# Kernel optimization log

Hardware: AMD Instinct MI355X
Metric: run time of the kernel (lower is better)

## Reference

```python
import jax, jax.numpy as jnp
import numpy as np

B, IN_DIM, N, L = 8, 2, 512, 64
D_MODEL = 32
D_FF = 32          # must equal D_MODEL: output_bn is BatchNorm2d(d_model) applied to skip
DEPTH = 3          # blocks=3 * layers=1; dilation resets to 1 each block -> all dilations = 1
KS = 2             # temporal kernel size
EPS = 1e-5         # BatchNorm eps


def setup_inputs() -> dict:
    key = jax.random.key(0)
    ks = jax.random.split(key, 16)
    s = 0.1  # weight scale for numeric sanity
    x = jax.random.normal(ks[0], (B, IN_DIM, N, L), jnp.float32)
    a = jax.random.uniform(ks[1], (N, N), jnp.float32)
    adj = a / a.sum(axis=1, keepdims=True)  # row-stochastic diffusion matrix
    return {
        "x": x,
        "adj": adj,
        "Wstart": jax.random.normal(ks[2], (D_MODEL, IN_DIM), jnp.float32) * s,
        "bstart": jnp.zeros((D_MODEL,), jnp.float32),
        "Wf": jax.random.normal(ks[3], (DEPTH, D_MODEL, D_MODEL, KS), jnp.float32) * s,
        "bf": jnp.zeros((DEPTH, D_MODEL), jnp.float32),
        "Wg": jax.random.normal(ks[4], (DEPTH, D_MODEL, D_MODEL, KS), jnp.float32) * s,
        "bg": jnp.zeros((DEPTH, D_MODEL), jnp.float32),
        "Wskip": jax.random.normal(ks[5], (DEPTH, D_FF, D_MODEL), jnp.float32) * s,
        "bskip": jnp.zeros((DEPTH, D_FF), jnp.float32),
        "Wgc": jax.random.normal(ks[6], (DEPTH, D_MODEL, 3 * D_MODEL), jnp.float32) * s,
        "bgc": jnp.zeros((DEPTH, D_MODEL), jnp.float32),
        "gcbn_g": jnp.ones((DEPTH, D_MODEL), jnp.float32),
        "gcbn_b": jnp.zeros((DEPTH, D_MODEL), jnp.float32),
        "bn_g": jnp.ones((DEPTH, D_MODEL), jnp.float32),
        "bn_b": jnp.zeros((DEPTH, D_MODEL), jnp.float32),
        "obn_g": jnp.ones((D_MODEL,), jnp.float32),
        "obn_b": jnp.zeros((D_MODEL,), jnp.float32),
    }


def _c1x1(x, W, b):
    # Conv2d with (1,1) kernel == channel mixing. x: [b,c,n,l], W: [o,c]
    return jnp.einsum('bcnl,oc->bonl', x, W) + b[None, :, None, None]


def _dconv(x, W, b, d):
    # Conv2d kernel (1,2), dilation d along time (valid). W: [o,c,2]
    Lx = x.shape[-1]
    y = (jnp.einsum('bcnl,oc->bonl', x[..., :Lx - d], W[..., 0])
         + jnp.einsum('bcnl,oc->bonl', x[..., d:], W[..., 1]))
    return y + b[None, :, None, None]


def _bn(x, g, bta):
    # eval-mode BatchNorm2d: running_mean=0, running_var=1
    inv = g / jnp.sqrt(1.0 + EPS)
    return x * inv[None, :, None, None] + bta[None, :, None, None]


def reference(x, adj, Wstart, bstart, Wf, bf, Wg, bg, Wskip, bskip,
              Wgc, bgc, gcbn_g, gcbn_b, bn_g, bn_b, obn_g, obn_b):
    rf = 1 + DEPTH * (KS - 1)  # receptive field with dilation 1 per layer
    h = _c1x1(x, Wstart, bstart)
    if h.shape[-1] < rf:
        h = jnp.pad(h, ((0, 0), (0, 0), (0, 0), (rf - h.shape[-1], 0)))
    skip = None
    for i in range(DEPTH):
        residual = h
        filt = jnp.tanh(_dconv(h, Wf[i], bf[i], 1))
        gate = jax.nn.sigmoid(_dconv(h, Wg[i], bg[i], 1))
        h = filt * gate
        s = _c1x1(h, Wskip[i], bskip[i])
        skip = s if skip is None else s + skip[..., -s.shape[-1]:]
        if i == DEPTH - 1:
            break
        # order-2 graph diffusion: h, A h, A^2 h -> concat -> 1x1 conv -> BN (dropout: eval noop)
        x1 = jnp.einsum('bcnl,nm->bcml', h, adj)
        x2 = jnp.einsum('bcnl,nm->bcml', x1, adj)
        cat = jnp.concatenate([h, x1, x2], axis=1)
        g = _bn(_c1x1(cat, Wgc[i], bgc[i]), gcbn_g[i], gcbn_b[i])
        h = g + residual[..., -g.shape[-1]:]
        h = _bn(h, bn_g[i], bn_b[i])
    out = _bn(skip, obn_g, obn_b)
    return jnp.swapaxes(out, 1, 3)  # [B, L', N, C]
```

## Files before the change

kernel.cpp:

```cpp
#include <hip/hip_runtime.h>
#include <hip/hip_bf16.h>

#define B_     8
#define CIN_   2
#define N_     512
#define C_     32
#define L_     64
#define LOUT_  61
#define BUF_   ((size_t)(8*32*512*64))

typedef __hip_bfloat16 bf16;
typedef unsigned short ushort_t;
typedef unsigned int u32;
typedef __attribute__((ext_vector_type(8))) unsigned short us8;
typedef __attribute__((ext_vector_type(8))) short bf16x8;
typedef __attribute__((ext_vector_type(4))) float f32x4;

static __device__ __forceinline__ float bits2f(ushort_t u) {
    return __uint_as_float(((unsigned)u) << 16);
}
static __device__ __forceinline__ ushort_t f2bits(float v) {
    unsigned u = __float_as_uint(v);
    return (ushort_t)((u + 0x7fffu + ((u >> 16) & 1u)) >> 16);
}

static __device__ __forceinline__ void gload16(const ushort_t* g, ushort_t* l) {
    __builtin_amdgcn_global_load_lds(
        (const __attribute__((address_space(1))) unsigned int*)g,
        (__attribute__((address_space(3))) unsigned int*)l,
        16, 0, 0);
}

static __device__ __forceinline__ u32 swap1(u32 v) {
    return (u32)__builtin_amdgcn_update_dpp(0, (int)v, 0xB1, 0xF, 0xF, true);
}

__global__ void k_start(const float* __restrict__ x,
                        const float* __restrict__ Wst,
                        const float* __restrict__ bst,
                        ushort_t* __restrict__ h) {
    int idx = blockIdx.x * 256 + threadIdx.x;
    int l0 = (idx & 7) * 8;
    int n  = (idx >> 3) & 511;
    int o  = (idx >> 12) & 31;
    int b  = idx >> 17;
    float w0 = Wst[o * 2], w1 = Wst[o * 2 + 1], bb = bst[o];
    int xbase = (b * CIN_ * N_ + n) * L_ + l0;
    float va[8], vb[8];
    *(float4*)&va[0] = *(const float4*)(x + xbase);
    *(float4*)&va[4] = *(const float4*)(x + xbase + 4);
    *(float4*)&vb[0] = *(const float4*)(x + xbase + N_ * L_);
    *(float4*)&vb[4] = *(const float4*)(x + xbase + N_ * L_ + 4);
    us8 r;
    #pragma unroll
    for (int k = 0; k < 8; ++k) r[k] = f2bits(bb + va[k] * w0 + vb[k] * w1);
    *(us8*)(h + (size_t)idx * 8) = r;
}

__global__ void k_transA(const float* __restrict__ adj, ushort_t* __restrict__ adjT) {
    __shared__ float buf[64][65];
    int ti = blockIdx.x & 7;
    int tj = blockIdx.x >> 3;
    int t = threadIdx.x;
    for (int r = 0; r < 16; ++r) {
        int e = t + 256 * r;
        int rl = e >> 6, cl = e & 63;
        buf[rl][cl] = adj[(size_t)(ti * 64 + rl) * 512 + tj * 64 + cl];
    }
    __syncthreads();
    for (int r = 0; r < 16; ++r) {
        int e = t + 256 * r;
        int ml = e >> 6, nl = e & 63;
        adjT[(size_t)(tj * 64 + ml) * 512 + ti * 64 + nl] = f2bits(buf[nl][ml]);
    }
}

__global__ __launch_bounds__(256, 2) void k_sq(const ushort_t* __restrict__ adjT,
                                               ushort_t* __restrict__ adj2T) {
    __shared__ __align__(16) ushort_t lds2[8192];
    ushort_t* As = lds2;
    ushort_t* Bs = lds2 + 4096;
    int mt = blockIdx.x & 7, nc = blockIdx.x >> 3;
    int t = threadIdx.x, lane = t & 63, w = t >> 6;
    int la = lane & 15, q = lane >> 4;
    f32x4 acc[4];
    #pragma unroll
    for (int mi = 0; mi < 4; ++mi) acc[mi] = (f32x4)0.f;
    for (int p0 = 0; p0 < 512; p0 += 64) {
        __syncthreads();
        #pragma unroll
        for (int r = 0; r < 2; ++r) {
            int e = t + 256 * r, ml = e >> 3, oct = e & 7;
            int sw = ((oct + (ml >> 3)) & 7) << 3;
            *(us8*)(As + ml * 64 + sw) =
                *(const us8*)(adjT + (size_t)(mt * 64 + ml) * 512 + p0 + oct * 8);
            *(us8*)(Bs + ml * 64 + sw) =
                *(const us8*)(adjT + (size_t)(p0 + ml) * 512 + nc * 64 + oct * 8);
        }
        __syncthreads();
        #pragma unroll
        for (int ks = 0; ks < 2; ++ks) {
            bf16x8 a[4];
            #pragma unroll
            for (int mi = 0; mi < 4; ++mi) {
                int m = mi * 16 + la;
                int bl = (ks * 4 + q + (m >> 3)) & 7;
                a[mi] = *(const bf16x8*)(As + m * 64 + bl * 8);
            }
            bf16x8 bv;
            {
                int n = w * 16 + la;
                int rot = ((n >> 3) + ks * 4 + q) & 7;
                int col = rot * 8 + (n & 7);
                const ushort_t* p = Bs + (ks * 32 + q * 8) * 64 + col;
                #pragma unroll
                for (int j = 0; j < 8; ++j) bv[j] = (short)p[j * 64];
            }
            #pragma unroll
            for (int mi = 0; mi < 4; ++mi)
                acc[mi] = __builtin_amdgcn_mfma_f32_16x16x32_bf16(a[mi], bv, acc[mi], 0, 0, 0);
        }
    }
    __syncthreads();
    ushort_t* Ys = lds2;
    #pragma unroll
    for (int mi = 0; mi < 4; ++mi)
        #pragma unroll
        for (int r = 0; r < 4; ++r)
            Ys[(mi * 16 + q * 4 + r) * 72 + w * 16 + la] = f2bits(acc[mi][r]);
    __syncthreads();
    #pragma unroll
    for (int r = 0; r < 2; ++r) {
        int e = t + 256 * r, ml = e >> 3, oct = e & 7;
        us8 v = *(const us8*)(Ys + ml * 72 + oct * 8);
        *(us8*)(adj2T + (size_t)(mt * 64 + ml) * 512 + nc * 64 + oct * 8) = v;
    }
}

__global__ __launch_bounds__(256, 2) void k_gs_mfma(
        const ushort_t* __restrict__ h,
        const float* __restrict__ Wf, const float* __restrict__ bfp,
        const float* __restrict__ Wg, const float* __restrict__ bgp,
        const float* __restrict__ Wsk, const float* __restrict__ bsk,
        ushort_t* __restrict__ G, float* __restrict__ out,
        int off, int mode, int storeG,
        const float* __restrict__ og, const float* __restrict__ obb) {
    __shared__ __align__(16) ushort_t Hs[128 * 72];
    __shared__ __align__(16) ushort_t Asf[32 * 72];
    __shared__ __align__(16) ushort_t Asg[32 * 72];
    __shared__ __align__(16) ushort_t As2[32 * 40];
    __shared__ float bfv[32], bgv[32], bsv[32];
    int t = threadIdx.x;
    int b = blockIdx.x >> 7, n0 = (blockIdx.x & 127) * 4;
    int lane = t & 63, w = t >> 6;
    int la = lane & 15, q = lane >> 4;

    {
        int o = t >> 3, k8 = (t & 7) * 8;
        us8 vf, vg;
        #pragma unroll
        for (int i = 0; i < 8; ++i) {
            int k = k8 + i, c = k & 31, tap = k >> 5;
            vf[i] = f2bits(Wf[o * 64 + c * 2 + tap]);
            vg[i] = f2bits(Wg[o * 64 + c * 2 + tap]);
        }
        *(us8*)(Asf + o * 72 + k8) = vf;
        *(us8*)(Asg + o * 72 + k8) = vg;
        if (k8 < 32) {
            us8 vs;
            #pragma unroll
            for (int i = 0; i < 8; ++i) vs[i] = f2bits(Wsk[o * 32 + k8 + i]);
            *(us8*)(As2 + o * 40 + k8) = vs;
        }
        if (t < 32) { bfv[t] = bfp[t]; bgv[t] = bgp[t]; bsv[t] = bsk[t]; }
    }
    const ushort_t* hb = h + (size_t)(b * 32) * 512 * 64;
    #pragma unroll
    for (int r = 0; r < 4; ++r) {
        int e = t + 256 * r;
        int row = e >> 3, oct = e & 7;
        us8 v = *(const us8*)(hb + ((size_t)(row >> 2) * 512 + n0 + (row & 3)) * 64 + oct * 8);
        int sw = (oct + row + (row >> 5)) & 7;
        *(us8*)(Hs + row * 72 + sw * 8) = v;
    }
    {
        int row = t >> 1, hf = t & 1;
        *(uint2*)(Hs + row * 72 + 64 + hf * 4) = make_uint2(0u, 0u);
    }
    __syncthreads();

    bf16x8 af[2][2], ag[2][2];
    #pragma unroll
    for (int mt = 0; mt < 2; ++mt)
        #pragma unroll
        for (int ks = 0; ks < 2; ++ks) {
            af[mt][ks] = *(const bf16x8*)(Asf + (mt * 16 + la) * 72 + ks * 32 + q * 8);
            ag[mt][ks] = *(const bf16x8*)(Asg + (mt * 16 + la) * 72 + ks * 32 + q * 8);
        }

    f32x4 fa[2][4], ga[2][4];
    #pragma unroll
    for (int mt = 0; mt < 2; ++mt)
        #pragma unroll
        for (int ct = 0; ct < 4; ++ct) { fa[mt][ct] = (f32x4)0.f; ga[mt][ct] = (f32x4)0.f; }
    #pragma unroll
    for (int ct = 0; ct < 4; ++ct) {
        #pragma unroll
        for (int ks = 0; ks < 2; ++ks) {
            int le = ct * 16 + la + ks;
            bf16x8 bv;
            #pragma unroll
            for (int j = 0; j < 8; ++j) {
                int row = 32 * q + 4 * j + w;
                int pos = (le < 64) ? ((((le >> 3) + row + q) & 7) * 8 + (le & 7)) : le;
                bv[j] = (short)Hs[row * 72 + pos];
            }
            #pragma unroll
            for (int mt = 0; mt < 2; ++mt) {
                fa[mt][ct] = __builtin_amdgcn_mfma_f32_16x16x32_bf16(af[mt][ks], bv, fa[mt][ct], 0, 0, 0);
                ga[mt][ct] = __builtin_amdgcn_mfma_f32_16x16x32_bf16(ag[mt][ks], bv, ga[mt][ct], 0, 0, 0);
            }
        }
    }

    #pragma unroll
    for (int mt = 0; mt < 2; ++mt)
        #pragma unroll
        for (int ct = 0; ct < 4; ++ct)
            #pragma unroll
            for (int r = 0; r < 4; ++r) {
                int o = mt * 16 + q * 4 + r;
                float fv = fa[mt][ct][r] + bfv[o];
                float gv = ga[mt][ct][r] + bgv[o];
                float ef = __expf(2.f * fv);
                float act = (1.f - 2.f / (ef + 1.f)) * (1.f / (1.f + __expf(-gv)));
                int l = ct * 16 + la;
                int row = o * 4 + w;
                int sw = ((l >> 3) + row + (row >> 5)) & 7;
                Hs[row * 72 + sw * 8 + (l & 7)] = f2bits(act);
            }

    bf16x8 a2[2];
    a2[0] = *(const bf16x8*)(As2 + la * 40 + q * 8);
    a2[1] = *(const bf16x8*)(As2 + (16 + la) * 40 + q * 8);
    f32x4 sa[2][4];
    #pragma unroll
    for (int mt = 0; mt < 2; ++mt)
        #pragma unroll
        for (int ct = 0; ct < 4; ++ct) sa[mt][ct] = (f32x4)0.f;
    #pragma unroll
    for (int ct = 0; ct < 4; ++ct) {
        int le = ct * 16 + la + off;
        bf16x8 bv;
        #pragma unroll
        for (int j = 0; j < 8; ++j) {
            int row = 32 * q + 4 * j + w;
            int pos = (le < 64) ? ((((le >> 3) + row + q) & 7) * 8 + (le & 7)) : le;
            bv[j] = (short)Hs[row * 72 + pos];
        }
        sa[0][ct] = __builtin_amdgcn_mfma_f32_16x16x32_bf16(a2[0], bv, sa[0][ct], 0, 0, 0);
        sa[1][ct] = __builtin_amdgcn_mfma_f32_16x16x32_bf16(a2[1], bv, sa[1][ct], 0, 0, 0);
    }
    __syncthreads();

    if (storeG) {
        #pragma unroll
        for (int r = 0; r < 4; ++r) {
            int e = t + 256 * r;
            int row = e >> 3, oct = e & 7;
            int sw = (oct + row + (row >> 5)) & 7;
            us8 v = *(const us8*)(Hs + row * 72 + sw * 8);
            *(us8*)(G + ((size_t)(b * 32 + (row >> 2)) * 512 + n0 + (row & 3)) * 64 + oct * 8) = v;
        }
    }
    __syncthreads();

    float* St = (float*)Hs;
    const float rbn = rsqrtf(1.f + 1e-5f);
    #pragma unroll
    for (int half = 0; half < 2; ++half) {
        if ((w >> 1) == half) {
            #pragma unroll
            for (int mt = 0; mt < 2; ++mt)
                #pragma unroll
                for (int ct = 0; ct < 4; ++ct) {
                    int col = (w & 1) * 64 + ct * 16 + la;
                    int ob = mt * 16 + q * 4;
                    float4 sv = make_float4(sa[mt][ct][0] + bsv[ob],
                                            sa[mt][ct][1] + bsv[ob + 1],
                                            sa[mt][ct][2] + bsv[ob + 2],
                                            sa[mt][ct][3] + bsv[ob + 3]);
                    *(float4*)(St + col * 36 + ob) = sv;
                }
        }
        __syncthreads();
        {
            int col = t >> 1, o0 = (t & 1) * 16;
            int nr = half * 2 + (col >> 6), l = col & 63;
            if (l < LOUT_) {
                float* po = out + ((size_t)(b * LOUT_ + l) * 512 + n0 + nr) * 32 + o0;
                #pragma unroll
                for (int i = 0; i < 4; ++i) {
                    float4 s = *(float4*)(St + col * 36 + o0 + i * 4);
                    if (mode == 0) {
                        *(float4*)(po + i * 4) = s;
                    } else {
                        float4 old = *(float4*)(po + i * 4);
                        float4 vv = make_float4(old.x + s.x, old.y + s.y,
                                                old.z + s.z, old.w + s.w);
                        if (mode == 2) {
                            int ob = o0 + i * 4;
                            vv.x = vv.x * (og[ob] * rbn) + obb[ob];
                            vv.y = vv.y * (og[ob + 1] * rbn) + obb[ob + 1];
                            vv.z = vv.z * (og[ob + 2] * rbn) + obb[ob + 2];
                            vv.w = vv.w * (og[ob + 3] * rbn) + obb[ob + 3];
                        }
                        *(float4*)(po + i * 4) = vv;
                    }
                }
            }
        }
        __syncthreads();
    }
}

__global__ __launch_bounds__(256, 2) void k_diffuse2(
        const ushort_t* __restrict__ X, const ushort_t* __restrict__ adjT,
        const ushort_t* __restrict__ adj2T,
        ushort_t* __restrict__ Y1, ushort_t* __restrict__ Y2) {
    __shared__ __align__(16) ushort_t lds[16384];
    ushort_t* As1 = lds;
    ushort_t* As2 = lds + 4096;
    ushort_t* Xs  = lds + 8192;
    int cp = blockIdx.x & 15;
    int mt = (blockIdx.x >> 4) & 7;
    int b  = blockIdx.x >> 7;
    int t  = threadIdx.x;
    int lane = t & 63, w = t >> 6;
    int c_loc = w & 1, lh = w >> 1;
    int m0 = mt * 64;
    int la = lane & 15, q = lane >> 4;
    int p_ = la & 1;
    u32 sel = p_ ? 0x07060302u : 0x05040100u;
    const ushort_t* Xb = X + (size_t)(b * 32 + cp * 2) * 512 * 64;
    f32x4 acc1[4][2], acc2[4][2];
    #pragma unroll
    for (int mi = 0; mi < 4; ++mi)
        #pragma unroll
        for (int li = 0; li < 2; ++li) { acc1[mi][li] = (f32x4)0.f; acc2[mi][li] = (f32x4)0.f; }

    union U { u32 u[4]; bf16x8 v; };

    for (int n0 = 0; n0 < 512; n0 += 64) {
        __syncthreads();
        #pragma unroll
        for (int r = 0; r < 2; ++r) {
            int e = t + 256 * r, ml = e >> 3, s = e & 7;
            int og = ((s - (ml >> 3)) & 7) * 8;
            gload16(adjT  + (size_t)(m0 + ml) * 512 + n0 + og, As1 + (size_t)e * 8);
            gload16(adj2T + (size_t)(m0 + ml) * 512 + n0 + og, As2 + (size_t)e * 8);
        }
        #pragma unroll
        for (int r = 0; r < 4; ++r) {
            int e = t + 256 * r;
            int cl = e >> 9, nl = (e >> 3) & 63, s = e & 7;
            int og = ((s - (nl >> 3)) & 7) * 8;
            gload16(Xb + ((size_t)cl * 512 + n0 + nl) * 64 + og, Xs + (size_t)e * 8);
        }
        __syncthreads();

        #pragma unroll
        for (int ks = 0; ks < 2; ++ks) {
            bf16x8 a1[4], a2v[4];
            #pragma unroll
            for (int mi = 0; mi < 4; ++mi) {
                int m = mi * 16 + la;
                int bl = (ks * 4 + q + (m >> 3)) & 7;
                a1[mi]  = *(const bf16x8*)(As1 + m * 64 + bl * 8);
                a2v[mi] = *(const bf16x8*)(As2 + m * 64 + bl * 8);
            }
            bf16x8 bb[2];
            #pragma unroll
            for (int li = 0; li < 2; ++li) {
                int l2 = lh * 32 + li * 16 + (la & ~1);
                int r0 = ks * 32 + q * 8 + p_ * 4;
                int rot = ((l2 >> 3) + ks * 4 + q) & 7;
                const u32* bp = (const u32*)(Xs + c_loc * 4096 + r0 * 64 + rot * 8 + (l2 & 7));
                u32 o0 = bp[0], o1 = bp[32], o2 = bp[64], o3 = bp[96];
                u32 s0 = swap1(o0), s1 = swap1(o1), s2 = swap1(o2), s3 = swap1(o3);
                u32 lo0 = p_ ? s0 : o0, lo1 = p_ ? s1 : o1;
                u32 lo2 = p_ ? s2 : o2, lo3 = p_ ? s3 : o3;
                u32 hi0 = p_ ? o0 : s0, hi1 = p_ ? o1 : s1;
                u32 hi2 = p_ ? o2 : s2, hi3 = p_ ? o3 : s3;
                U u;
                u.u[0] = __builtin_amdgcn_perm(lo1, lo0, sel);
                u.u[1] = __builtin_amdgcn_perm(lo3, lo2, sel);
                u.u[2] = __builtin_amdgcn_perm(hi1, hi0, sel);
                u.u[3] = __builtin_amdgcn_perm(hi3, hi2, sel);
                bb[li] = u.v;
            }
            #pragma unroll
            for (int mi = 0; mi < 4; ++mi)
                #pragma unroll
                for (int li = 0; li < 2; ++li) {
                    acc1[mi][li] = __builtin_amdgcn_mfma_f32_16x16x32_bf16(a1[mi],  bb[li], acc1[mi][li], 0, 0, 0);
                    acc2[mi][li] = __builtin_amdgcn_mfma_f32_16x16x32_bf16(a2v[mi], bb[li], acc2[mi][li], 0, 0, 0);
                }
        }
    }
    ushort_t* Ys = lds;
    #pragma unroll
    for (int pass = 0; pass < 2; ++pass) {
        __syncthreads();
        f32x4 (*src)[2] = pass ? acc2 : acc1;
        #pragma unroll
        for (int mi = 0; mi < 4; ++mi)
            #pragma unroll
            for (int li = 0; li < 2; ++li)
                #pragma unroll
                for (int r = 0; r < 4; ++r) {
                    int row = mi * 16 + q * 4 + r;
                    int col = lh * 32 + li * 16 + la;
                    Ys[c_loc * 4608 + row * 72 + col] = f2bits(src[mi][li][r]);
                }
        __syncthreads();
        ushort_t* Yo = pass ? Y2 : Y1;
        int c = t >> 7, mrem = t & 127;
        int m = mrem >> 1, lq = mrem & 1;
        #pragma unroll
        for (int r = 0; r < 4; ++r) {
            int l0 = lq * 32 + r * 8;
            us8 v = *(const us8*)(Ys + c * 4608 + m * 72 + l0);
            *(us8*)(Yo + ((size_t)(b * 32 + cp * 2 + c) * 512 + m0 + m) * 64 + l0) = v;
        }
    }
}

__global__ __launch_bounds__(256, 2) void k_gc3_mfma(
        ushort_t* __restrict__ G, const ushort_t* __restrict__ X1,
        const ushort_t* __restrict__ X2, const ushort_t* __restrict__ hres,
        const float* __restrict__ Wgc, const float* __restrict__ bgc,
        const float* __restrict__ gg, const float* __restrict__ gb,
        const float* __restrict__ bg2, const float* __restrict__ bb2) {
    __shared__ __align__(16) ushort_t cat[384 * 72];
    __shared__ __align__(16) ushort_t hr[128 * 64];
    __shared__ __align__(16) ushort_t Aw[32 * 104];
    __shared__ float prm[5][32];
    int t = threadIdx.x;
    int b = blockIdx.x >> 7, n0 = (blockIdx.x & 127) * 4;
    int lane = t & 63, w = t >> 6;
    int la = lane & 15, q = lane >> 4;

    #pragma unroll
    for (int r = 0; r < 12; ++r) {
        int e = t + 256 * r;
        int row = e >> 3, oct = e & 7;
        int k = row >> 2;
        const ushort_t* src = (k < 32) ? G : ((k < 64) ? X1 : X2);
        us8 v = *(const us8*)(src + ((size_t)(b * 32 + (k & 31)) * 512 + n0 + (row & 3)) * 64 + oct * 8);
        int sw = (oct + row + (row >> 5)) & 7;
        *(us8*)(cat + row * 72 + sw * 8) = v;
    }
    #pragma unroll
    for (int r = 0; r < 4; ++r) {
        int e = t + 256 * r;
        int row = e >> 3, oct = e & 7;
        us8 v = *(const us8*)(hres + ((size_t)(b * 32 + (row >> 2)) * 512 + n0 + (row & 3)) * 64 + oct * 8);
        *(us8*)(hr + row * 64 + oct * 8) = v;
    }
    for (int e = t; e < 384; e += 256) {
        int o = e / 12, oct = e % 12;
        us8 v;
        #pragma unroll
        for (int i = 0; i < 8; ++i) v[i] = f2bits(Wgc[o * 96 + oct * 8 + i]);
        *(us8*)(Aw + o * 104 + oct * 8) = v;
    }
    if (t < 32) {
        prm[0][t] = bgc[t]; prm[1][t] = gg[t]; prm[2][t] = gb[t];
        prm[3][t] = bg2[t]; prm[4][t] = bb2[t];
    }
    __syncthreads();

    bf16x8 a[2][3];
    #pragma unroll
    for (int mt = 0; mt < 2; ++mt)
        #pragma unroll
        for (int ks = 0; ks < 3; ++ks)
            a[mt][ks] = *(const bf16x8*)(Aw + (mt * 16 + la) * 104 + ks * 32 + q * 8);

    f32x4 acc[2][4];
    #pragma unroll
    for (int mt = 0; mt < 2; ++mt)
        #pragma unroll
        for (int ct = 0; ct < 4; ++ct) acc[mt][ct] = (f32x4)0.f;
    #pragma unroll
    for (int ct = 0; ct < 4; ++ct) {
        int le = ct * 16 + la;
        #pragma unroll
        for (int ks = 0; ks < 3; ++ks) {
            bf16x8 bv;
            #pragma unroll
            for (int j = 0; j < 8; ++j) {
                int row = (ks * 32 + q * 8 + j) * 4 + w;
                int sw = ((le >> 3) + row + (row >> 5)) & 7;
                bv[j] = (short)cat[row * 72 + sw * 8 + (le & 7)];
            }
            acc[0][ct] = __builtin_amdgcn_mfma_f32_16x16x32_bf16(a[0][ks], bv, acc[0][ct], 0, 0, 0);
            acc[1][ct] = __builtin_amdgcn_mfma_f32_16x16x32_bf16(a[1][ks], bv, acc[1][ct], 0, 0, 0);
        }
    }
    __syncthreads();

    const float rbn = rsqrtf(1.f + 1e-5f);
    #pragma unroll
    for (int mt = 0; mt < 2; ++mt)
        #pragma unroll
        for (int ct = 0; ct < 4; ++ct)
            #pragma unroll
            for (int r = 0; r < 4; ++r) {
                int o = mt * 16 + q * 4 + r;
                int l = ct * 16 + la;
                float v = acc[mt][ct][r] + prm[0][o];
                v = v * (prm[1][o] * rbn) + prm[2][o];
                float res = (l < 63) ? bits2f(hr[(o * 4 + w) * 64 + l + 1]) : 0.f;
                v = (v + res) * (prm[3][o] * rbn) + prm[4][o];
                int row = o * 4 + w;
                int sw = ((l >> 3) + row + (row >> 5)) & 7;
                cat[row * 72 + sw * 8 + (l & 7)] = f2bits(v);
            }
    __syncthreads();
    #pragma unroll
    for (int r = 0; r < 4; ++r) {
        int e = t + 256 * r;
        int row = e >> 3, oct = e & 7;
        int sw = (oct + row + (row >> 5)) & 7;
        us8 v = *(const us8*)(cat + row * 72 + sw * 8);
        *(us8*)(G + ((size_t)(b * 32 + (row >> 2)) * 512 + n0 + (row & 3)) * 64 + oct * 8) = v;
    }
}

extern "C" void kernel_launch(void* const* d_in, const int* in_sizes, int n_in,
                              void* d_out, int out_size, void* d_ws, size_t ws_size,
                              hipStream_t stream) {
    const float* x      = (const float*)d_in[0];
    const float* adj    = (const float*)d_in[1];
    const float* Wstart = (const float*)d_in[2];
    const float* bstart = (const float*)d_in[3];
    const float* Wf     = (const float*)d_in[4];
    const float* bf_    = (const float*)d_in[5];
    const float* Wg     = (const float*)d_in[6];
    const float* bg     = (const float*)d_in[7];
    const float* Wskip  = (const float*)d_in[8];
    const float* bskip  = (const float*)d_in[9];
    const float* Wgc    = (const float*)d_in[10];
    const float* bgc    = (const float*)d_in[11];
    const float* gcbn_g = (const float*)d_in[12];
    const float* gcbn_b = (const float*)d_in[13];
    const float* bn_g   = (const float*)d_in[14];
    const float* bn_b   = (const float*)d_in[15];
    const float* obn_g  = (const float*)d_in[16];
    const float* obn_b  = (const float*)d_in[17];
    float* out = (float*)d_out;

    ushort_t* P0    = (ushort_t*)d_ws;
    ushort_t* P1    = P0 + BUF_;
    ushort_t* P2    = P1 + BUF_;
    ushort_t* P3    = P2 + BUF_;
    ushort_t* adjT  = P3 + BUF_;
    ushort_t* adj2T = adjT + 512 * 512;

    k_transA<<<64, 256, 0, stream>>>(adj, adjT);
    k_sq<<<64, 256, 0, stream>>>(adjT, adj2T);
    k_start<<<4096, 256, 0, stream>>>(x, Wstart, bstart, P0);

    ushort_t* h  = P0;
    ushort_t* Gb = P1;
    for (int i = 0; i < 3; ++i) {
        int mode = (i == 0) ? 0 : ((i == 2) ? 2 : 1);
        k_gs_mfma<<<1024, 256, 0, stream>>>(h, Wf + i * 2048, bf_ + i * 32,
                                            Wg + i * 2048, bg + i * 32,
                                            Wskip + i * 1024, bskip + i * 32,
                                            Gb, out, 2 - i, mode, (i < 2) ? 1 : 0,
                                            obn_g, obn_b);
        if (i == 2) break;
        k_diffuse2<<<1024, 256, 0, stream>>>(Gb, adjT, adj2T, P2, P3);
        k_gc3_mfma<<<1024, 256, 0, stream>>>(Gb, P2, P3, h,
                                             Wgc + i * 3072, bgc + i * 32,
                                             gcbn_g + i * 32, gcbn_b + i * 32,
                                             bn_g + i * 32, bn_b + i * 32);
        ushort_t* tmp = h; h = Gb; Gb = tmp;
    }
}
```

Measured before the change: 317.4 us.

## Double-buffer LDS tiles in diffusion kernel and re-swizzle X layout

Doubles the LDS allocation in k_diffuse2 so the next n-chunk of adjT, adj2T and X is prefetched while MFMAs run on the current chunk, leaving one barrier per iteration instead of two. It also changes the X tile swizzle to rotate by row as well as row-block, so the four per-row u32 B-operand reads hit different banks. The larger LDS footprint (64KB per block) may limit the two-blocks-per-CU occupancy the launch bounds request.

```diff
diff --git a/kernel.cpp b/kernel.cpp
--- a/kernel.cpp
+++ b/kernel.cpp
@@ -328,10 +328,7 @@
         const ushort_t* __restrict__ X, const ushort_t* __restrict__ adjT,
         const ushort_t* __restrict__ adj2T,
         ushort_t* __restrict__ Y1, ushort_t* __restrict__ Y2) {
-    __shared__ __align__(16) ushort_t lds[16384];
-    ushort_t* As1 = lds;
-    ushort_t* As2 = lds + 4096;
-    ushort_t* Xs  = lds + 8192;
+    __shared__ __align__(16) ushort_t lds[32768];
     int cp = blockIdx.x & 15;
     int mt = (blockIdx.x >> 4) & 7;
     int b  = blockIdx.x >> 7;
@@ -351,24 +348,36 @@
 
     union U { u32 u[4]; bf16x8 v; };
 
-    for (int n0 = 0; n0 < 512; n0 += 64) {
-        __syncthreads();
+    auto STAGE = [&](int n0, ushort_t* bb) {
+        ushort_t* As1b = bb;
+        ushort_t* As2b = bb + 4096;
+        ushort_t* Xsb  = bb + 8192;
         #pragma unroll
         for (int r = 0; r < 2; ++r) {
             int e = t + 256 * r, ml = e >> 3, s = e & 7;
             int og = ((s - (ml >> 3)) & 7) * 8;
-            gload16(adjT  + (size_t)(m0 + ml) * 512 + n0 + og, As1 + (size_t)e * 8);
-            gload16(adj2T + (size_t)(m0 + ml) * 512 + n0 + og, As2 + (size_t)e * 8);
+            gload16(adjT  + (size_t)(m0 + ml) * 512 + n0 + og, As1b + (size_t)e * 8);
+            gload16(adj2T + (size_t)(m0 + ml) * 512 + n0 + og, As2b + (size_t)e * 8);
         }
         #pragma unroll
         for (int r = 0; r < 4; ++r) {
             int e = t + 256 * r;
             int cl = e >> 9, nl = (e >> 3) & 63, s = e & 7;
-            int og = ((s - (nl >> 3)) & 7) * 8;
-            gload16(Xb + ((size_t)cl * 512 + n0 + nl) * 64 + og, Xs + (size_t)e * 8);
-        }
-        __syncthreads();
-
+            int og = ((s - nl - (nl >> 3)) & 7) * 8;
+            gload16(Xb + ((size_t)cl * 512 + n0 + nl) * 64 + og, Xsb + (size_t)e * 8);
+        }
+    };
+
+    STAGE(0, lds);
+    __syncthreads();
+
+    for (int it = 0; it < 8; ++it) {
+        ushort_t* cur = lds + (it & 1) * 16384;
+        if (it < 7) STAGE((it + 1) * 64, lds + ((it + 1) & 1) * 16384);
+        ushort_t* As1 = cur;
+        ushort_t* As2 = cur + 4096;
+        ushort_t* Xs  = cur + 8192;
+        const ushort_t* xc = Xs + c_loc * 4096;
         #pragma unroll
         for (int ks = 0; ks < 2; ++ks) {
             bf16x8 a1[4], a2v[4];
@@ -384,9 +393,11 @@
             for (int li = 0; li < 2; ++li) {
                 int l2 = lh * 32 + li * 16 + (la & ~1);
                 int r0 = ks * 32 + q * 8 + p_ * 4;
-                int rot = ((l2 >> 3) + ks * 4 + q) & 7;
-                const u32* bp = (const u32*)(Xs + c_loc * 4096 + r0 * 64 + rot * 8 + (l2 & 7));
-                u32 o0 = bp[0], o1 = bp[32], o2 = bp[64], o3 = bp[96];
+                int brot = ((l2 >> 3) + p_ * 4 + ks * 4 + q) & 7;
+                u32 o0 = *(const u32*)(xc + (r0 + 0) * 64 + (((brot + 0) & 7) << 3) + (l2 & 7));
+                u32 o1 = *(const u32*)(xc + (r0 + 1) * 64 + (((brot + 1) & 7) << 3) + (l2 & 7));
+                u32 o2 = *(const u32*)(xc + (r0 + 2) * 64 + (((brot + 2) & 7) << 3) + (l2 & 7));
+                u32 o3 = *(const u32*)(xc + (r0 + 3) * 64 + (((brot + 3) & 7) << 3) + (l2 & 7));
                 u32 s0 = swap1(o0), s1 = swap1(o1), s2 = swap1(o2), s3 = swap1(o3);
                 u32 lo0 = p_ ? s0 : o0, lo1 = p_ ? s1 : o1;
                 u32 lo2 = p_ ? s2 : o2, lo3 = p_ ? s3 : o3;
@@ -407,7 +418,9 @@
                     acc2[mi][li] = __builtin_amdgcn_mfma_f32_16x16x32_bf16(a2v[mi], bb[li], acc2[mi][li], 0, 0, 0);
                 }
         }
-    }
+        __syncthreads();
+    }
+
     ushort_t* Ys = lds;
     #pragma unroll
     for (int pass = 0; pass < 2; ++pass) {
```

Measured after the change: 308.9 us. 1.03x faster.
